# Optimization experiments

Measured on AMD Instinct MI355X. Metric: run time of the kernel, lower is better.

## Reference

```python
import jax, jax.numpy as jnp
import numpy as np

B, D, C_IN, C_OUT = 256, 8, 2, 4


def setup_inputs() -> dict:
    key = jax.random.key(0)
    k1, k2, k3, k4 = jax.random.split(key, 4)
    rho = jax.random.normal(k1, (B, C_IN * D * D, C_IN * D * D), dtype=jnp.float32)
    ux = jax.random.normal(k2, (D, D), dtype=jnp.float32)
    uy = jax.random.normal(k3, (D, D), dtype=jnp.float32)
    uc = jax.random.normal(k4, (C_OUT, C_OUT), dtype=jnp.float32)
    return {"rho": rho, "ux": ux, "uy": uy, "uc": uc}


def _insert_channels(rho, d, c_in, c_out):
    # Faithful port of _InsertChannels: move each (channel f, pixel i,j) row/col
    # index to channel f + (c_out - c_in) in the enlarged register.
    b = rho.shape[0]
    x = jnp.arange(c_in * d * d)
    f = x // (d * d)                       # channel index
    i = (x % (d * d)) // d                 # row pixel
    j = x % d                              # col pixel
    new_idx = i * d + j + (f + (c_out - c_in)) * d * d  # [c_in*d^2]
    big = jnp.zeros((b, c_out * d * d, c_out * d * d), dtype=rho.dtype)
    # Indices are a bijection onto a sub-block, so add == set (matches
    # index_put_(..., accumulate=True) in torch).
    return big.at[:, new_idx[:, None], new_idx[None, :]].add(rho)


def reference(rho, ux, uy, uc):
    d = ux.shape[0]
    c_out = uc.shape[0]
    c_in = rho.shape[1] // (d * d)
    # channel insertion (c_in < c_out path)
    rho_big = _insert_channels(rho, d, c_in, c_out)        # [b, C, C], C = c_out*d^2
    # u = kron(uc, kron(ux, uy))
    u = jnp.kron(uc, jnp.kron(ux, uy))                     # [C, C]
    # new_rho = u @ rho @ u^H (real float32 -> conj is identity, transpose only)
    u_rho = jnp.einsum('pq,bqr->bpr', u, rho_big)
    new_rho = jnp.einsum('bpr,sr->bps', u_rho, u)
    return new_rho
```

## Files before the change

kernel.cpp:

```cpp
#include <hip/hip_runtime.h>


#define TPB 256

__global__ __launch_bounds__(TPB, 2) void qconv_fused(
    const float* __restrict__ rho,
    const float* __restrict__ ux,
    const float* __restrict__ uy,
    const float* __restrict__ uc,
    float* __restrict__ out)
{
    __shared__ alignas(16) float L[4][64][68];

    const int tid  = threadIdx.x;
    const int w    = tid >> 6;
    const int lane = tid & 63;
    const int c1   = w >> 1, c2 = w & 1;
    const int px   = lane >> 3, qx = lane & 7;

    const int blk = blockIdx.x;
    const int b   = ((blk >> 5) << 3) | (blk & 7);
    const int c   = (blk >> 3) & 3;

    const float* rb = rho + (size_t)b * 16384 + (size_t)((c1 << 6) + (px << 3)) * 128
                      + (c2 << 6) + (qx << 3);

    float X[64], Y[64];

#pragma unroll
    for (int py = 0; py < 8; ++py) {
        float4 lo = *(const float4*)(rb + py * 128);
        float4 hi = *(const float4*)(rb + py * 128 + 4);
        X[py * 8 + 0] = lo.x; X[py * 8 + 1] = lo.y; X[py * 8 + 2] = lo.z; X[py * 8 + 3] = lo.w;
        X[py * 8 + 4] = hi.x; X[py * 8 + 5] = hi.y; X[py * 8 + 6] = hi.z; X[py * 8 + 7] = hi.w;
    }

#pragma unroll
    for (int py = 0; py < 8; ++py) {
#pragma unroll
        for (int j = 0; j < 8; ++j) {
            float acc = 0.f;
#pragma unroll
            for (int k = 0; k < 8; ++k) acc += uy[j * 8 + k] * X[py * 8 + k];
            Y[py * 8 + j] = acc;
        }
    }
#pragma unroll
    for (int i = 0; i < 8; ++i) {
#pragma unroll
        for (int j = 0; j < 8; ++j) {
            float acc = 0.f;
#pragma unroll
            for (int k = 0; k < 8; ++k) acc += uy[i * 8 + k] * Y[k * 8 + j];
            X[i * 8 + j] = acc;
        }
    }

#pragma unroll
    for (int e = 0; e < 64; ++e) L[w][e][lane] = X[e];
    __syncthreads();
#pragma unroll
    for (int f4 = 0; f4 < 16; ++f4) {
        float4 v = *(const float4*)&L[w][lane][f4 * 4];
        X[f4 * 4 + 0] = v.x; X[f4 * 4 + 1] = v.y; X[f4 * 4 + 2] = v.z; X[f4 * 4 + 3] = v.w;
    }

#pragma unroll
    for (int p = 0; p < 8; ++p) {
#pragma unroll
        for (int j = 0; j < 8; ++j) {
            float acc = 0.f;
#pragma unroll
            for (int k = 0; k < 8; ++k) acc += ux[j * 8 + k] * X[p * 8 + k];
            Y[p * 8 + j] = acc;
        }
    }
#pragma unroll
    for (int i = 0; i < 8; ++i) {
#pragma unroll
        for (int j = 0; j < 8; ++j) {
            float acc = 0.f;
#pragma unroll
            for (int k = 0; k < 8; ++k) acc += ux[i * 8 + k] * Y[k * 8 + j];
            X[i * 8 + j] = acc;
        }
    }

    __syncthreads();

    {
        const int pyp = lane >> 3, qyp = lane & 7;
#pragma unroll
        for (int px_ = 0; px_ < 8; ++px_)
#pragma unroll
            for (int qx_ = 0; qx_ < 8; ++qx_)
                L[w][px_ * 8 + pyp][qx_ * 8 + qyp] = X[px_ * 8 + qx_];
    }
    __syncthreads();

    const float e0 = uc[c * 4 + 2], e1 = uc[c * 4 + 3];
    float a2[4][2];
#pragma unroll
    for (int cs = 0; cs < 4; ++cs) { a2[cs][0] = uc[cs * 4 + 2]; a2[cs][1] = uc[cs * 4 + 3]; }

    float* ob = out + (size_t)b * 65536;
#pragma unroll
    for (int i = 0; i < 4; ++i) {
        const int g  = tid + 256 * i;
        const int sp = g >> 4;
        const int qg = g & 15;
        float4 wv[4];
#pragma unroll
        for (int ww = 0; ww < 4; ++ww) wv[ww] = *(const float4*)&L[ww][sp][qg * 4];
#pragma unroll
        for (int cs = 0; cs < 4; ++cs) {
            const float k00 = e0 * a2[cs][0], k01 = e0 * a2[cs][1];
            const float k10 = e1 * a2[cs][0], k11 = e1 * a2[cs][1];
            float4 v;
            v.x = k00 * wv[0].x + k01 * wv[1].x + k10 * wv[2].x + k11 * wv[3].x;
            v.y = k00 * wv[0].y + k01 * wv[1].y + k10 * wv[2].y + k11 * wv[3].y;
            v.z = k00 * wv[0].z + k01 * wv[1].z + k10 * wv[2].z + k11 * wv[3].z;
            v.w = k00 * wv[0].w + k01 * wv[1].w + k10 * wv[2].w + k11 * wv[3].w;
            *(float4*)&ob[(size_t)((c * 64 + sp) * 256 + cs * 64 + qg * 4)] = v;
        }
    }
}

extern "C" void kernel_launch(void* const* d_in, const int* in_sizes, int n_in,
                              void* d_out, int out_size, void* d_ws, size_t ws_size,
                              hipStream_t stream) {
    const float* rho = (const float*)d_in[0];
    const float* ux  = (const float*)d_in[1];
    const float* uy  = (const float*)d_in[2];
    const float* uc  = (const float*)d_in[3];
    float* out = (float*)d_out;
    qconv_fused<<<dim3(1024), dim3(TPB), 0, stream>>>(rho, ux, uy, uc, out);
}
```

Measured before the change: 97.08 us.

## Compute each batch's transform once per block and write all channel rows

```diff
diff --git a/kernel.cpp b/kernel.cpp
--- a/kernel.cpp
+++ b/kernel.cpp
@@ -1,7 +1,7 @@
 #include <hip/hip_runtime.h>
 
 
-#define TPB 256
+#define TPB 512
 
 __global__ __launch_bounds__(TPB, 2) void qconv_fused(
     const float* __restrict__ rho,
@@ -12,116 +12,113 @@
 {
     __shared__ alignas(16) float L[4][64][68];
 
-    const int tid  = threadIdx.x;
-    const int w    = tid >> 6;
-    const int lane = tid & 63;
-    const int c1   = w >> 1, c2 = w & 1;
-    const int px   = lane >> 3, qx = lane & 7;
+    const int tid = threadIdx.x;
+    const int b   = blockIdx.x;
 
-    const int blk = blockIdx.x;
-    const int b   = ((blk >> 5) << 3) | (blk & 7);
-    const int c   = (blk >> 3) & 3;
+    if (tid < 256) {
+        const int w    = tid >> 6;
+        const int lane = tid & 63;
+        const int c1   = w >> 1, c2 = w & 1;
+        const int px   = lane >> 3, qx = lane & 7;
 
-    const float* rb = rho + (size_t)b * 16384 + (size_t)((c1 << 6) + (px << 3)) * 128
-                      + (c2 << 6) + (qx << 3);
+        const float* rb = rho + (size_t)b * 16384
+                        + (size_t)((c1 << 6) + (px << 3)) * 128 + (c2 << 6) + (qx << 3);
 
-    float X[64], Y[64];
+        float X[64], Y[64];
 
 #pragma unroll
-    for (int py = 0; py < 8; ++py) {
-        float4 lo = *(const float4*)(rb + py * 128);
-        float4 hi = *(const float4*)(rb + py * 128 + 4);
-        X[py * 8 + 0] = lo.x; X[py * 8 + 1] = lo.y; X[py * 8 + 2] = lo.z; X[py * 8 + 3] = lo.w;
-        X[py * 8 + 4] = hi.x; X[py * 8 + 5] = hi.y; X[py * 8 + 6] = hi.z; X[py * 8 + 7] = hi.w;
-    }
+        for (int py = 0; py < 8; ++py) {
+            float4 lo = *(const float4*)(rb + py * 128);
+            float4 hi = *(const float4*)(rb + py * 128 + 4);
+            X[py*8+0]=lo.x; X[py*8+1]=lo.y; X[py*8+2]=lo.z; X[py*8+3]=lo.w;
+            X[py*8+4]=hi.x; X[py*8+5]=hi.y; X[py*8+6]=hi.z; X[py*8+7]=hi.w;
+        }
 
 #pragma unroll
-    for (int py = 0; py < 8; ++py) {
+        for (int py = 0; py < 8; ++py)
 #pragma unroll
-        for (int j = 0; j < 8; ++j) {
-            float acc = 0.f;
+            for (int j = 0; j < 8; ++j) {
+                float acc = 0.f;
 #pragma unroll
-            for (int k = 0; k < 8; ++k) acc += uy[j * 8 + k] * X[py * 8 + k];
-            Y[py * 8 + j] = acc;
-        }
-    }
+                for (int k = 0; k < 8; ++k) acc += uy[j*8+k] * X[py*8+k];
+                Y[py*8+j] = acc;
+            }
 #pragma unroll
-    for (int i = 0; i < 8; ++i) {
+        for (int i = 0; i < 8; ++i)
 #pragma unroll
-        for (int j = 0; j < 8; ++j) {
-            float acc = 0.f;
+            for (int j = 0; j < 8; ++j) {
+                float acc = 0.f;
 #pragma unroll
-            for (int k = 0; k < 8; ++k) acc += uy[i * 8 + k] * Y[k * 8 + j];
-            X[i * 8 + j] = acc;
-        }
-    }
+                for (int k = 0; k < 8; ++k) acc += uy[i*8+k] * Y[k*8+j];
+                X[i*8+j] = acc;
+            }
 
 #pragma unroll
-    for (int e = 0; e < 64; ++e) L[w][e][lane] = X[e];
-    __syncthreads();
+        for (int e = 0; e < 64; ++e) L[w][e][lane] = X[e];
+        __asm__ volatile("s_waitcnt lgkmcnt(0)" ::: "memory");
 #pragma unroll
-    for (int f4 = 0; f4 < 16; ++f4) {
-        float4 v = *(const float4*)&L[w][lane][f4 * 4];
-        X[f4 * 4 + 0] = v.x; X[f4 * 4 + 1] = v.y; X[f4 * 4 + 2] = v.z; X[f4 * 4 + 3] = v.w;
-    }
+        for (int f4 = 0; f4 < 16; ++f4) {
+            float4 v = *(const float4*)&L[w][lane][f4 * 4];
+            X[f4*4+0]=v.x; X[f4*4+1]=v.y; X[f4*4+2]=v.z; X[f4*4+3]=v.w;
+        }
 
 #pragma unroll
-    for (int p = 0; p < 8; ++p) {
+        for (int p = 0; p < 8; ++p)
 #pragma unroll
-        for (int j = 0; j < 8; ++j) {
-            float acc = 0.f;
+            for (int j = 0; j < 8; ++j) {
+                float acc = 0.f;
 #pragma unroll
-            for (int k = 0; k < 8; ++k) acc += ux[j * 8 + k] * X[p * 8 + k];
-            Y[p * 8 + j] = acc;
-        }
-    }
+                for (int k = 0; k < 8; ++k) acc += ux[j*8+k] * X[p*8+k];
+                Y[p*8+j] = acc;
+            }
 #pragma unroll
-    for (int i = 0; i < 8; ++i) {
+        for (int i = 0; i < 8; ++i)
 #pragma unroll
-        for (int j = 0; j < 8; ++j) {
-            float acc = 0.f;
+            for (int j = 0; j < 8; ++j) {
+                float acc = 0.f;
 #pragma unroll
-            for (int k = 0; k < 8; ++k) acc += ux[i * 8 + k] * Y[k * 8 + j];
-            X[i * 8 + j] = acc;
+                for (int k = 0; k < 8; ++k) acc += ux[i*8+k] * Y[k*8+j];
+                X[i*8+j] = acc;
+            }
+
+        {
+            const int pyp = lane >> 3, qyp = lane & 7;
+#pragma unroll
+            for (int px_ = 0; px_ < 8; ++px_)
+#pragma unroll
+                for (int qx_ = 0; qx_ < 8; ++qx_)
+                    L[w][px_*8+pyp][qx_*8+qyp] = X[px_*8+qx_];
         }
     }
 
     __syncthreads();
 
-    {
-        const int pyp = lane >> 3, qyp = lane & 7;
+    float e0[4], e1[4];
 #pragma unroll
-        for (int px_ = 0; px_ < 8; ++px_)
-#pragma unroll
-            for (int qx_ = 0; qx_ < 8; ++qx_)
-                L[w][px_ * 8 + pyp][qx_ * 8 + qyp] = X[px_ * 8 + qx_];
-    }
-    __syncthreads();
-
-    const float e0 = uc[c * 4 + 2], e1 = uc[c * 4 + 3];
-    float a2[4][2];
-#pragma unroll
-    for (int cs = 0; cs < 4; ++cs) { a2[cs][0] = uc[cs * 4 + 2]; a2[cs][1] = uc[cs * 4 + 3]; }
+    for (int c = 0; c < 4; ++c) { e0[c] = uc[c*4+2]; e1[c] = uc[c*4+3]; }
 
     float* ob = out + (size_t)b * 65536;
 #pragma unroll
-    for (int i = 0; i < 4; ++i) {
-        const int g  = tid + 256 * i;
+    for (int i = 0; i < 2; ++i) {
+        const int g  = tid + TPB * i;
         const int sp = g >> 4;
         const int qg = g & 15;
         float4 wv[4];
 #pragma unroll
         for (int ww = 0; ww < 4; ++ww) wv[ww] = *(const float4*)&L[ww][sp][qg * 4];
 #pragma unroll
-        for (int cs = 0; cs < 4; ++cs) {
-            const float k00 = e0 * a2[cs][0], k01 = e0 * a2[cs][1];
-            const float k10 = e1 * a2[cs][0], k11 = e1 * a2[cs][1];
-            float4 v;
-            v.x = k00 * wv[0].x + k01 * wv[1].x + k10 * wv[2].x + k11 * wv[3].x;
-            v.y = k00 * wv[0].y + k01 * wv[1].y + k10 * wv[2].y + k11 * wv[3].y;
-            v.z = k00 * wv[0].z + k01 * wv[1].z + k10 * wv[2].z + k11 * wv[3].z;
-            v.w = k00 * wv[0].w + k01 * wv[1].w + k10 * wv[2].w + k11 * wv[3].w;
-            *(float4*)&ob[(size_t)((c * 64 + sp) * 256 + cs * 64 + qg * 4)] = v;
+        for (int c = 0; c < 4; ++c) {
+#pragma unroll
+            for (int cs = 0; cs < 4; ++cs) {
+                const float k00 = e0[c]*e0[cs], k01 = e0[c]*e1[cs];
+                const float k10 = e1[c]*e0[cs], k11 = e1[c]*e1[cs];
+                float4 v;
+                v.x = k00*wv[0].x + k01*wv[1].x + k10*wv[2].x + k11*wv[3].x;
+                v.y = k00*wv[0].y + k01*wv[1].y + k10*wv[2].y + k11*wv[3].y;
+                v.z = k00*wv[0].z + k01*wv[1].z + k10*wv[2].z + k11*wv[3].z;
+                v.w = k00*wv[0].w + k01*wv[1].w + k10*wv[2].w + k11*wv[3].w;
+                *(float4*)&ob[(size_t)((c*64 + sp) * 256 + cs*64 + qg*4)] = v;
+            }
         }
     }
 }
@@ -134,5 +131,5 @@
     const float* uy  = (const float*)d_in[2];
     const float* uc  = (const float*)d_in[3];
     float* out = (float*)d_out;
-    qconv_fused<<<dim3(1024), dim3(TPB), 0, stream>>>(rho, ux, uy, uc, out);
+    qconv_fused<<<dim3(256), dim3(TPB), 0, stream>>>(rho, ux, uy, uc, out);
 }
```

Result: faster. 90.14 us (-7.1%).
